# Kernel tuning notes

Hardware: AMD Instinct MI355X
Metric: run time of the kernel (lower is better)

The kernel has to match this reference:

```python
import jax, jax.numpy as jnp
import numpy as np


def _cofactor_antieq(M):
    """ith output = M[...,i,0] * (-1)**i * det(M with row i and col 0 deleted).

    M: (..., n, n) -> (..., n). Vectorized form of the original per-row
    jnp.delete + stack + det construction.
    """
    n = M.shape[-1]
    # rows[i] = all row indices except i, shape (n, n-1)
    rows = np.stack([np.delete(np.arange(n), i) for i in range(n)])
    Msub = M[..., 1:]                 # delete first column: (..., n, n-1)
    sub = Msub[..., rows, :]          # delete row i per output: (..., n, n-1, n-1)
    signs = jnp.asarray((-1.0) ** np.arange(n), dtype=M.dtype)
    return M[..., 0] * signs * jnp.linalg.det(sub)


def setup_inputs() -> dict:
    key = jax.random.key(0)
    ks = jax.random.split(key, 6)
    B, NSPIN, NPS, D, NION, DIM = 4096, 2, 16, 256, 8, 3
    eq_inputs = jax.random.normal(ks[0], (B, NSPIN * NPS, D), jnp.float32)
    r_ei = jax.random.normal(ks[1], (B, NSPIN * NPS, NION, DIM), jnp.float32)
    # per-spin linear orbital params (stacked over spin since splits are equal)
    W = jax.random.normal(ks[2], (NSPIN, D, NPS), jnp.float32) / np.sqrt(D)
    b = jax.random.normal(ks[3], (NSPIN, NPS), jnp.float32) * 0.01
    # anisotropic envelope decay matrices A per (spin, ion, orbital), near identity
    env_dim = jax.random.normal(ks[4], (NSPIN, NION, NPS, DIM, DIM), jnp.float32) * 0.1 + jnp.eye(DIM, dtype=jnp.float32)
    # linear combination over ions per (spin, orbital)
    env_ion = jax.random.normal(ks[5], (NSPIN, NION, NPS), jnp.float32) / NION
    return dict(eq_inputs=eq_inputs, r_ei=r_ei, W=W, b=b, env_dim=env_dim, env_ion=env_ion)


def reference(eq_inputs, r_ei, W, b, env_dim, env_ion):
    B = eq_inputs.shape[0]
    nspin, d, nps = W.shape
    nion, dim = r_ei.shape[-2], r_ei.shape[-1]
    # split particles by spin: (B, nspin, nps, ...)
    xs = eq_inputs.reshape(B, nspin, nps, d)
    rs = r_ei.reshape(B, nspin, nps, nion, dim)
    # linear part of orbitals: (B, s, n, o) with n = o = nps (square per spin)
    y = jnp.einsum('bsnd,sdo->bsno', xs, W) + b[:, None, :]
    # anisotropic exponential envelope: exp(-||A (r - R)||), summed over ions
    Ar = jnp.einsum('sioed,bsnid->bsnioe', env_dim, rs)        # (B,s,n,ion,orb,3)
    env = jnp.einsum('bsnio,sio->bsno',
                     jnp.exp(-jnp.linalg.norm(Ar, axis=-1)), env_ion)
    M = y * env                                                 # (B, s, n, n)
    cof = _cofactor_antieq(M)                                   # (B, s, n)
    return cof[..., None]                                       # (B, s, n, 1)
```

## Files before the change

kernel.cpp:

```cpp
#include <hip/hip_runtime.h>
#include <math.h>


__global__ __launch_bounds__(256)
void cof_matrix(const float* __restrict__ eq,
                const float* __restrict__ rei,
                const float* __restrict__ Wm,
                const float* __restrict__ bb,
                const float* __restrict__ edim,
                const float* __restrict__ eion,
                float* __restrict__ ws)
{
  __shared__ __align__(16) float Wp[4096];
  __shared__ __align__(16) float Gl[8 * 6 * 16];
  __shared__ __align__(16) float Xs[4][2][1024];

  const int tid   = threadIdx.x;
  const int lane  = tid & 63;
  const int wv    = tid >> 6;
  const int blk   = blockIdx.x;
  const int sp    = blk >> 10;
  const int bbase = (blk & 1023) * 4;

  const float* wb = Wm + (size_t)sp * 4096;

  #pragma unroll
  for (int t = 0; t < 4; ++t) {
    const int idx = t * 256 + tid;
    ((float4*)Wp)[idx] = ((const float4*)wb)[idx];
  }

  if (tid < 128) {
    const int i = tid >> 4, o = tid & 15;
    const float* A = edim + (((size_t)sp * 8 + i) * 16 + o) * 9;
    const float a0=A[0],a1=A[1],a2=A[2],a3=A[3],a4=A[4],a5=A[5],a6=A[6],a7=A[7],a8=A[8];
    float* Gp = Gl + i * 96 + o;
    Gp[0]  = a0*a0 + a3*a3 + a6*a6;
    Gp[16] = a1*a1 + a4*a4 + a7*a7;
    Gp[32] = a2*a2 + a5*a5 + a8*a8;
    Gp[48] = 2.f*(a0*a1 + a3*a4 + a6*a7);
    Gp[64] = 2.f*(a0*a2 + a3*a5 + a6*a8);
    Gp[80] = 2.f*(a1*a2 + a4*a5 + a7*a8);
  }
  __syncthreads();

  const int bidx = bbase + wv;
  const int cch  = lane >> 4;
  const int nb   = (lane >> 2) & 3;
  const int ob   = lane & 3;

  const float* xb = eq + ((size_t)bidx * 32 + sp * 16) * 256;

  const int srow = lane >> 4;
  const int schk = lane & 15;

  float* xw0 = &Xs[wv][0][0];
  float* xw1 = &Xs[wv][1][0];

  float acc[4][4] = {{0.f,0.f,0.f,0.f},{0.f,0.f,0.f,0.f},
                     {0.f,0.f,0.f,0.f},{0.f,0.f,0.f,0.f}};

  float4 sA[4], sB[4];

#define LOADQ(dst, qq)                                                        \
  _Pragma("unroll")                                                           \
  for (int t = 0; t < 4; ++t)                                                 \
    dst[t] = *(const float4*)(xb + (4 * t + srow) * 256 + (qq) * 64 + schk * 4);

#define WRITEQ(buf, src)                                                      \
  _Pragma("unroll")                                                           \
  for (int t = 0; t < 4; ++t) {                                               \
    const int row_ = 4 * t + srow;                                            \
    *(float4*)((buf) + row_ * 64 + ((schk ^ row_) << 2)) = src[t];            \
  }

#define COMPQ(buf, qq)                                                        \
  _Pragma("unroll")                                                           \
  for (int g = 0; g < 4; ++g) {                                               \
    const int dg = (qq) * 64 + g * 16 + cch * 4;                              \
    float xr[4][4], wr4[4][4];                                                \
    _Pragma("unroll")                                                         \
    for (int r = 0; r < 4; ++r) {                                             \
      const int R_ = 4 * nb + r;                                              \
      float4 t = *(const float4*)((buf) + R_ * 64 +                           \
                                  (((g * 4 + cch) ^ R_) << 2));               \
      xr[r][0]=t.x; xr[r][1]=t.y; xr[r][2]=t.z; xr[r][3]=t.w;                 \
    }                                                                         \
    _Pragma("unroll")                                                         \
    for (int j = 0; j < 4; ++j) {                                             \
      float4 t = *(const float4*)(Wp + (dg + j) * 16 + 4 * ob);               \
      wr4[j][0]=t.x; wr4[j][1]=t.y; wr4[j][2]=t.z; wr4[j][3]=t.w;             \
    }                                                                         \
    _Pragma("unroll")                                                         \
    for (int r = 0; r < 4; ++r)                                               \
      _Pragma("unroll")                                                       \
      for (int j = 0; j < 4; ++j)                                             \
        _Pragma("unroll")                                                     \
        for (int c2 = 0; c2 < 4; ++c2)                                        \
          acc[r][c2] = fmaf(xr[r][j], wr4[j][c2], acc[r][c2]);                \
  }

  LOADQ(sA, 0)
  WRITEQ(xw0, sA)
  LOADQ(sB, 1)
  COMPQ(xw0, 0)
  WRITEQ(xw1, sB)
  LOADQ(sA, 2)
  COMPQ(xw1, 1)
  WRITEQ(xw0, sA)
  LOADQ(sB, 3)
  COMPQ(xw0, 2)
  WRITEQ(xw1, sB)
  COMPQ(xw1, 3)

#undef LOADQ
#undef WRITEQ
#undef COMPQ

  #pragma unroll
  for (int r = 0; r < 4; ++r)
    #pragma unroll
    for (int c2 = 0; c2 < 4; ++c2) {
      float v = acc[r][c2];
      v += __shfl_xor(v, 16);
      v += __shfl_xor(v, 32);
      acc[r][c2] = v;
    }

  float* Mw = xw0;
  {
    float4 bv = *(const float4*)(bb + sp * 16 + 4 * ob);
    if (lane < 16) {
      #pragma unroll
      for (int r = 0; r < 4; ++r) {
        float4 v = make_float4(acc[r][0] + bv.x, acc[r][1] + bv.y,
                               acc[r][2] + bv.z, acc[r][3] + bv.w);
        *(float4*)(Mw + (4 * nb + r) * 20 + 4 * ob) = v;
      }
    }
  }

  {
    const int n = lane >> 2;
    const float* rp = rei + ((size_t)bidx * 32 + sp * 16 + n) * 24;
    float rv[24];
    #pragma unroll
    for (int t4 = 0; t4 < 6; ++t4) {
      float4 t = *(const float4*)(rp + t4 * 4);
      rv[t4*4+0]=t.x; rv[t4*4+1]=t.y; rv[t4*4+2]=t.z; rv[t4*4+3]=t.w;
    }
    float4 env = make_float4(0.f, 0.f, 0.f, 0.f);
    #pragma unroll
    for (int i = 0; i < 8; ++i) {
      const float r0 = rv[i*3], r1 = rv[i*3+1], r2 = rv[i*3+2];
      const float rr0 = r0*r0, rr1 = r1*r1, rr2 = r2*r2;
      const float rr3 = r0*r1, rr4 = r0*r2, rr5 = r1*r2;
      const float* Gp = Gl + i * 96 + 4 * ob;
      const float4 q00 = *(const float4*)(Gp);
      const float4 q11 = *(const float4*)(Gp + 16);
      const float4 q22 = *(const float4*)(Gp + 32);
      const float4 q01 = *(const float4*)(Gp + 48);
      const float4 q02 = *(const float4*)(Gp + 64);
      const float4 q12 = *(const float4*)(Gp + 80);
      const float4 io  = *(const float4*)(eion + ((size_t)sp * 8 + i) * 16 + 4 * ob);
#define ENVC(c) { float n2 = q00.c*rr0 + q11.c*rr1 + q22.c*rr2 \
                           + q01.c*rr3 + q02.c*rr4 + q12.c*rr5; \
                  n2 = fmaxf(n2, 0.f); \
                  env.c += __expf(-sqrtf(n2)) * io.c; }
      ENVC(x) ENVC(y) ENVC(z) ENVC(w)
#undef ENVC
    }
    const float* mp = Mw + n * 20 + 4 * ob;
    float4 y = *(const float4*)mp;
    const size_t pair = (size_t)bidx * 2 + sp;
    *(float4*)(ws + pair * 256 + n * 16 + 4 * ob) =
        make_float4(y.x * env.x, y.y * env.y, y.z * env.z, y.w * env.w);
  }
}

__global__ __launch_bounds__(64)
void cof_lu(const float* __restrict__ ws,
            float* __restrict__ out)
{
  const int lane = threadIdx.x;
  const int g  = lane >> 4;
  const int r  = lane & 15;
  const int gb = lane & 48;
  const size_t pair = (size_t)blockIdx.x * 4 + g;
  const float* mg = ws + pair * 256;

  float a[16];
  #pragma unroll
  for (int c = 0; c < 16; ++c) a[c] = mg[c * 16 + r];

  float det = 1.0f;
  int sign = 0;
  unsigned retired = 0;
  unsigned pp0 = 0, pp1 = 0;
  int srr = 0;
  float accf = (r == 0) ? 1.0f : 0.0f;
  float acc2 = 0.0f;

  #pragma unroll
  for (int k = 0; k < 16; ++k) {
    const bool act = ((retired >> r) & 1u) == 0u;
    const float av = act ? fabsf(a[k]) : 0.0f;
    unsigned pk = (__float_as_uint(av) & 0xFFFFFFF0u) | (unsigned)r;
    #pragma unroll
    for (int m = 1; m <= 8; m <<= 1) {
      unsigned o2 = __shfl_xor(pk, m);
      pk = (pk > o2) ? pk : o2;
    }
    const int p = (int)(pk & 15u);
    if (k < 8) pp0 |= (unsigned)p << (4 * k);
    else       pp1 |= (unsigned)p << (4 * (k - 8));
    float pv = __shfl(a[k], gb | p);
    if (fabsf(pv) < 1e-30f) pv = (pv < 0.0f) ? -1e-30f : 1e-30f;
    det *= pv;
    retired |= (1u << p);
    sign ^= (int)(__popc((~retired) & ((1u << p) - 1u)) & 1u);
    if (r == p) srr = k;
    const bool upd = act && (r != p);
    float m2 = 0.0f;
    if (upd) { m2 = a[k] / pv; a[k] = m2; }
    #pragma unroll
    for (int c = k + 1; c < 16; ++c) {
      float bcv = __shfl(a[c], gb | p);
      if (upd) a[c] = fmaf(-m2, bcv, a[c]);
    }
    float zk = __shfl(accf, gb | p);
    if (r == p) acc2 = zk;
    if (upd) accf = fmaf(-m2, zk, accf);
  }
  if (sign) det = -det;

  float myx = 0.0f;
  #pragma unroll
  for (int j = 15; j >= 0; --j) {
    float t = acc2 / a[j];
    const int pj = (int)(((j >= 8) ? (pp1 >> (4 * (j - 8)))
                                   : (pp0 >> (4 * j))) & 15u);
    float xj = __shfl(t, gb | pj);
    if (srr < j) acc2 = fmaf(-a[j], xj, acc2);
    if (r == j) myx = xj;
  }

  const float mi0 = mg[r * 16];
  out[pair * 16 + r] = mi0 * det * myx;
}

extern "C" void kernel_launch(void* const* d_in, const int* in_sizes, int n_in,
                              void* d_out, int out_size, void* d_ws, size_t ws_size,
                              hipStream_t stream) {
  (void)in_sizes; (void)n_in; (void)out_size; (void)ws_size;
  const float* eq   = (const float*)d_in[0];
  const float* rei  = (const float*)d_in[1];
  const float* Wm   = (const float*)d_in[2];
  const float* bb   = (const float*)d_in[3];
  const float* edim = (const float*)d_in[4];
  const float* eion = (const float*)d_in[5];
  float* out = (float*)d_out;
  float* ws  = (float*)d_ws;
  hipLaunchKernelGGL(cof_matrix, dim3(2048), dim3(256), 0, stream,
                     eq, rei, Wm, bb, edim, eion, ws);
  hipLaunchKernelGGL(cof_lu, dim3(2048), dim3(64), 0, stream, ws, out);
}
```

Measured before the change: 224.6 us.

## Stream X tiles to LDS with direct global-to-LDS loads and pad W

Replaces the register-staged global load plus LDS write of each X quarter with global_load_lds direct DMA into a swizzled LDS layout. Double buffering is now governed by explicit vmcnt waits and scheduling barriers. The W table is padded to a stride of 20 to reduce LDS bank conflicts, and the M scratch area moves to its own buffer so it no longer aliases an X buffer. This frees VGPRs and removes the LDS store instructions, at the cost of more LDS space and a fragile, hand-counted wait scheme.

After: 228.1 us. About the same (+1.6%).

```diff
diff --git a/kernel.cpp b/kernel.cpp
--- a/kernel.cpp
+++ b/kernel.cpp
@@ -1,6 +1,11 @@
 #include <hip/hip_runtime.h>
 #include <math.h>
 
+
+#define GLOAD_LDS16(gp, lp)                                                   \
+  __builtin_amdgcn_global_load_lds(                                           \
+      (const __attribute__((address_space(1))) void*)(gp),                    \
+      (__attribute__((address_space(3))) void*)(lp), 16, 0, 0)
 
 __global__ __launch_bounds__(256)
 void cof_matrix(const float* __restrict__ eq,
@@ -11,9 +16,10 @@
                 const float* __restrict__ eion,
                 float* __restrict__ ws)
 {
-  __shared__ __align__(16) float Wp[4096];
+  __shared__ __align__(16) float Wp[256 * 20];
   __shared__ __align__(16) float Gl[8 * 6 * 16];
   __shared__ __align__(16) float Xs[4][2][1024];
+  __shared__ __align__(16) float Ml[4 * 320];
 
   const int tid   = threadIdx.x;
   const int lane  = tid & 63;
@@ -27,7 +33,10 @@
   #pragma unroll
   for (int t = 0; t < 4; ++t) {
     const int idx = t * 256 + tid;
-    ((float4*)Wp)[idx] = ((const float4*)wb)[idx];
+    const int d   = idx >> 2;
+    const int c4  = idx & 3;
+    float4 v = ((const float4*)wb)[idx];
+    *(float4*)(Wp + d * 20 + c4 * 4) = v;
   }
 
   if (tid < 128) {
@@ -48,48 +57,44 @@
   const int cch  = lane >> 4;
   const int nb   = (lane >> 2) & 3;
   const int ob   = lane & 3;
+  const int rl   = lane >> 4;
+  const int sl   = lane & 15;
 
   const float* xb = eq + ((size_t)bidx * 32 + sp * 16) * 256;
 
-  const int srow = lane >> 4;
-  const int schk = lane & 15;
-
-  float* xw0 = &Xs[wv][0][0];
-  float* xw1 = &Xs[wv][1][0];
+  float* xwA = &Xs[wv][0][0];
+  float* xwB = &Xs[wv][1][0];
 
   float acc[4][4] = {{0.f,0.f,0.f,0.f},{0.f,0.f,0.f,0.f},
                      {0.f,0.f,0.f,0.f},{0.f,0.f,0.f,0.f}};
 
-  float4 sA[4], sB[4];
-
-#define LOADQ(dst, qq)                                                        \
+#define STAGEQ(bufp, qt)                                                      \
+  { _Pragma("unroll")                                                         \
+    for (int i = 0; i < 4; ++i) {                                             \
+      const int R_ = 4 * i + rl;                                              \
+      const float* src_ = xb + (size_t)R_ * 256 + (qt) * 64                   \
+                          + ((sl ^ (R_ & 7)) * 4);                            \
+      GLOAD_LDS16(src_, (bufp) + i * 256);                                    \
+    } }
+
+#define COMPQ(bufp, qt)                                                       \
   _Pragma("unroll")                                                           \
-  for (int t = 0; t < 4; ++t)                                                 \
-    dst[t] = *(const float4*)(xb + (4 * t + srow) * 256 + (qq) * 64 + schk * 4);
-
-#define WRITEQ(buf, src)                                                      \
-  _Pragma("unroll")                                                           \
-  for (int t = 0; t < 4; ++t) {                                               \
-    const int row_ = 4 * t + srow;                                            \
-    *(float4*)((buf) + row_ * 64 + ((schk ^ row_) << 2)) = src[t];            \
-  }
-
-#define COMPQ(buf, qq)                                                        \
-  _Pragma("unroll")                                                           \
-  for (int g = 0; g < 4; ++g) {                                               \
-    const int dg = (qq) * 64 + g * 16 + cch * 4;                              \
-    float xr[4][4], wr4[4][4];                                                \
+  for (int qq = 0; qq < 4; ++qq) {                                            \
+    const int q  = (qt) * 4 + qq;                                             \
+    const int dg = q * 16 + cch * 4;                                          \
+    float wr4[4][4];                                                          \
+    _Pragma("unroll")                                                         \
+    for (int j = 0; j < 4; ++j) {                                             \
+      float4 t = *(const float4*)(Wp + (dg + j) * 20 + 4 * ob);               \
+      wr4[j][0]=t.x; wr4[j][1]=t.y; wr4[j][2]=t.z; wr4[j][3]=t.w;             \
+    }                                                                         \
+    float xr[4][4];                                                           \
     _Pragma("unroll")                                                         \
     for (int r = 0; r < 4; ++r) {                                             \
       const int R_ = 4 * nb + r;                                              \
-      float4 t = *(const float4*)((buf) + R_ * 64 +                           \
-                                  (((g * 4 + cch) ^ R_) << 2));               \
+      const int ck = (qq * 4 + cch) ^ (R_ & 7);                               \
+      float4 t = *(const float4*)((bufp) + R_ * 64 + ck * 4);                 \
       xr[r][0]=t.x; xr[r][1]=t.y; xr[r][2]=t.z; xr[r][3]=t.w;                 \
-    }                                                                         \
-    _Pragma("unroll")                                                         \
-    for (int j = 0; j < 4; ++j) {                                             \
-      float4 t = *(const float4*)(Wp + (dg + j) * 16 + 4 * ob);               \
-      wr4[j][0]=t.x; wr4[j][1]=t.y; wr4[j][2]=t.z; wr4[j][3]=t.w;             \
     }                                                                         \
     _Pragma("unroll")                                                         \
     for (int r = 0; r < 4; ++r)                                               \
@@ -100,21 +105,24 @@
           acc[r][c2] = fmaf(xr[r][j], wr4[j][c2], acc[r][c2]);                \
   }
 
-  LOADQ(sA, 0)
-  WRITEQ(xw0, sA)
-  LOADQ(sB, 1)
-  COMPQ(xw0, 0)
-  WRITEQ(xw1, sB)
-  LOADQ(sA, 2)
-  COMPQ(xw1, 1)
-  WRITEQ(xw0, sA)
-  LOADQ(sB, 3)
-  COMPQ(xw0, 2)
-  WRITEQ(xw1, sB)
-  COMPQ(xw1, 3)
-
-#undef LOADQ
-#undef WRITEQ
+  STAGEQ(xwA, 0)
+  STAGEQ(xwB, 1)
+  asm volatile("s_waitcnt vmcnt(4)" ::: "memory");
+  __builtin_amdgcn_sched_barrier(0);
+  COMPQ(xwA, 0)
+  STAGEQ(xwA, 2)
+  asm volatile("s_waitcnt vmcnt(4)" ::: "memory");
+  __builtin_amdgcn_sched_barrier(0);
+  COMPQ(xwB, 1)
+  STAGEQ(xwB, 3)
+  asm volatile("s_waitcnt vmcnt(4)" ::: "memory");
+  __builtin_amdgcn_sched_barrier(0);
+  COMPQ(xwA, 2)
+  asm volatile("s_waitcnt vmcnt(0)" ::: "memory");
+  __builtin_amdgcn_sched_barrier(0);
+  COMPQ(xwB, 3)
+
+#undef STAGEQ
 #undef COMPQ
 
   #pragma unroll
@@ -127,7 +135,7 @@
       acc[r][c2] = v;
     }
 
-  float* Mw = xw0;
+  float* Mw = Ml + wv * 320;
   {
     float4 bv = *(const float4*)(bb + sp * 16 + 4 * ob);
     if (lane < 16) {
```
